# Optimization experiments

Hardware: AMD Instinct MI355X
Metric: run time of the kernel (lower is better)

Reference implementation:

```python
import jax, jax.numpy as jnp
import numpy as np

B, S, D = 64, 1024, 800      # batch, seq_len, encoder hidden (2*hidden_dim, bidirectional)
MS, T = 16, 32               # max slots (spans) per sample, max span length
H = 200                      # LSTM hidden per direction = trs_hidden_dim // 2
NS = 12                      # number of slot names in the domain


def setup_inputs() -> dict:
    key = jax.random.key(0)
    ks = jax.random.split(key, 13)
    s = 0.05
    return {
        "hidden_layers": jax.random.normal(ks[0], (B, S, D), jnp.float32),
        "Wih_f": jax.random.normal(ks[1], (4 * H, D), jnp.float32) * s,
        "Whh_f": jax.random.normal(ks[2], (4 * H, H), jnp.float32) * s,
        "bih_f": jax.random.normal(ks[3], (4 * H,), jnp.float32) * s,
        "bhh_f": jax.random.normal(ks[4], (4 * H,), jnp.float32) * s,
        "Wih_b": jax.random.normal(ks[5], (4 * H, D), jnp.float32) * s,
        "Whh_b": jax.random.normal(ks[6], (4 * H, H), jnp.float32) * s,
        "bih_b": jax.random.normal(ks[7], (4 * H,), jnp.float32) * s,
        "bhh_b": jax.random.normal(ks[8], (4 * H,), jnp.float32) * s,
        "slot_embs": jax.random.normal(ks[9], (2 * H, NS), jnp.float32) * s,
        "span_starts": jnp.sort(jax.random.randint(ks[10], (B, MS), 0, S - T), axis=-1),
        "span_lens": jax.random.randint(ks[11], (B, MS), 1, T + 1),
        "slot_mask": jnp.ones((B, MS), jnp.float32),
    }


def _lstm_scan(x, m, Wih, Whh, bih, bhh):
    """Masked unidirectional LSTM. x: [N,T,Din], m: [N,T] bool-ish. Returns [N,T,H]."""
    N = x.shape[0]
    bias = bih + bhh

    def step(carry, xm):
        h, c = carry
        xt, mt = xm
        z = xt @ Wih.T + h @ Whh.T + bias            # [N, 4H], PyTorch gate order i,f,g,o
        i, f, g, o = jnp.split(z, 4, axis=-1)
        c_new = jax.nn.sigmoid(f) * c + jax.nn.sigmoid(i) * jnp.tanh(g)
        h_new = jax.nn.sigmoid(o) * jnp.tanh(c_new)
        mm = mt[:, None]
        h = jnp.where(mm, h_new, h)                  # freeze state on padded steps
        c = jnp.where(mm, c_new, c)
        return (h, c), h

    h0 = jnp.zeros((N, H), x.dtype)
    (_, _), hs = jax.lax.scan(step, (h0, h0), (jnp.swapaxes(x, 0, 1), m.T.astype(bool)))
    return jnp.swapaxes(hs, 0, 1)


def reference(hidden_layers, Wih_f, Whh_f, bih_f, bhh_f, Wih_b, Whh_b, bih_b, bhh_b,
              slot_embs, span_starts, span_lens, slot_mask):
    Bv, Sv, Dv = hidden_layers.shape
    # Padded ragged span gather: [B, MS, T]
    idx = jnp.clip(span_starts[..., None] + jnp.arange(T), 0, Sv - 1)
    tok_mask = (jnp.arange(T)[None, None, :] < span_lens[..., None]).astype(hidden_layers.dtype)
    spans = hidden_layers[jnp.arange(Bv)[:, None, None], idx]      # [B, MS, T, D]

    x = spans.reshape(Bv * MS, T, Dv)
    m = tok_mask.reshape(Bv * MS, T)
    h_f = _lstm_scan(x, m, Wih_f, Whh_f, bih_f, bhh_f)             # forward direction
    h_b = _lstm_scan(x[:, ::-1], m[:, ::-1], Wih_b, Whh_b, bih_b, bhh_b)[:, ::-1]
    y = jnp.concatenate([h_f, h_b], axis=-1)                       # [N, T, 2H]

    feats = jnp.sum(y * m[..., None], axis=1).reshape(Bv, MS, 2 * H)  # sum over span tokens
    logits = jnp.einsum('bmh,hn->bmn', feats, slot_embs)           # slot-name scores
    return logits * slot_mask[..., None]
```

## Files before the change

### kernel.cpp

```cpp
#include <hip/hip_runtime.h>


typedef __attribute__((ext_vector_type(4))) float f32x4;
typedef __attribute__((ext_vector_type(8))) short s16x8;

__device__ __forceinline__ unsigned short f2bf(float f) {
    union { float f; unsigned int u; } a; a.f = f;
    unsigned int u = a.u;
    u += 0x7fffu + ((u >> 16) & 1u);
    return (unsigned short)(u >> 16);
}
__device__ __forceinline__ float bf2f(unsigned short s) {
    union { unsigned int u; float f; } a; a.u = ((unsigned int)s) << 16; return a.f;
}
__device__ __forceinline__ void async_copy16(const void* g, void* l) {
    __builtin_amdgcn_global_load_lds(
        (const __attribute__((address_space(1))) unsigned int*)g,
        (__attribute__((address_space(3))) unsigned int*)l, 16, 0, 0);
}
__device__ __forceinline__ float sigf_(float x) {
    return 1.f / (1.f + __expf(-x));
}
__device__ __forceinline__ float tanhf_(float x) {
    float ax = fabsf(x);
    float e = __expf(-2.f * ax);
    float r = (1.f - e) / (1.f + e);
    return x < 0.f ? -r : r;
}

__global__ void pack_kernel(const float* __restrict__ Wih_f, const float* __restrict__ Wih_b,
                            const float* __restrict__ Whh_f, const float* __restrict__ Whh_b,
                            const float* __restrict__ bih_f, const float* __restrict__ bhh_f,
                            const float* __restrict__ bih_b, const float* __restrict__ bhh_b,
                            unsigned short* __restrict__ Wp, unsigned short* __restrict__ WhhP,
                            float* __restrict__ biasP)
{
    int tid = blockIdx.x * blockDim.x + threadIdx.x;
    if (tid < 1664 * 800) {
        int n = tid / 800, k = tid - n * 800;
        float v = 0.f;
        if (n < 800)       v = Wih_f[n * 800 + k];
        else if (n < 1600) v = Wih_b[(n - 800) * 800 + k];
        Wp[tid] = f2bf(v);
        return;
    }
    int t2 = tid - 1664 * 800;
    if (t2 < 1600 * 224) {
        int n = t2 / 224, k = t2 - n * 224;
        float v = 0.f;
        if (k < 200) v = (n < 800) ? Whh_f[n * 200 + k] : Whh_b[(n - 800) * 200 + k];
        WhhP[t2] = f2bf(v);
        return;
    }
    int t3 = t2 - 1600 * 224;
    if (t3 < 1664) {
        float v = 0.f;
        if (t3 < 800)       v = bih_f[t3] + bhh_f[t3];
        else if (t3 < 1600) v = bih_b[t3 - 800] + bhh_b[t3 - 800];
        biasP[t3] = v;
    }
}

__global__ void gather_kernel(const float* __restrict__ hidden, const int* __restrict__ starts,
                              unsigned short* __restrict__ Xg)
{
    int tid = blockIdx.x * blockDim.x + threadIdx.x;
    if (tid >= 32768 * 200) return;
    int row = tid / 200;
    int c4  = tid - row * 200;
    int t   = row >> 10, seq = row & 1023;
    int b   = seq >> 4;
    int src = starts[seq] + t;
    src = src < 1023 ? src : 1023;
    const float4 v = *(const float4*)(hidden + (size_t)(b * 1024 + src) * 800 + c4 * 4);
    ushort4 o;
    o.x = f2bf(v.x); o.y = f2bf(v.y); o.z = f2bf(v.z); o.w = f2bf(v.w);
    *(ushort4*)(Xg + (size_t)row * 800 + c4 * 4) = o;
}

__global__ __launch_bounds__(256) void gemm_kernel(const unsigned short* __restrict__ Xg,
                                                   const unsigned short* __restrict__ Wp,
                                                   const float* __restrict__ biasP,
                                                   unsigned short* __restrict__ Zf,
                                                   unsigned short* __restrict__ Zb)
{
    __shared__ __align__(16) unsigned short As[128 * 32];
    __shared__ __align__(16) unsigned short Bs[128 * 32];
    const int tid = threadIdx.x;
    const int wid = tid >> 6, lane = tid & 63;
    const int m0 = blockIdx.x * 128;
    const int n0 = blockIdx.y * 128;
    const int wm = (wid >> 1) * 64, wn = (wid & 1) * 64;
    const int l15 = lane & 15, l4 = lane >> 4;

    f32x4 acc[4][4];
#pragma unroll
    for (int i = 0; i < 4; i++)
#pragma unroll
        for (int j = 0; j < 4; j++) acc[i][j] = (f32x4){0.f, 0.f, 0.f, 0.f};

    const int r0 = tid >> 2,         kc0 = (tid & 3) * 8;
    const int r1 = (256 + tid) >> 2, kc1 = (tid & 3) * 8;
    unsigned short* AsB0 = As + (size_t)(wid * 64) * 8;
    unsigned short* AsB1 = As + (size_t)(256 + wid * 64) * 8;
    unsigned short* BsB0 = Bs + (size_t)(wid * 64) * 8;
    unsigned short* BsB1 = Bs + (size_t)(256 + wid * 64) * 8;

    for (int kb = 0; kb < 25; ++kb) {
        const int kk = kb * 32;
        async_copy16(Xg + (size_t)(m0 + r0) * 800 + kk + kc0, AsB0);
        async_copy16(Xg + (size_t)(m0 + r1) * 800 + kk + kc1, AsB1);
        async_copy16(Wp + (size_t)(n0 + r0) * 800 + kk + kc0, BsB0);
        async_copy16(Wp + (size_t)(n0 + r1) * 800 + kk + kc1, BsB1);
        __syncthreads();

        s16x8 a[4], b[4];
#pragma unroll
        for (int i = 0; i < 4; i++)
            a[i] = *(const s16x8*)(As + (wm + i * 16 + l15) * 32 + l4 * 8);
#pragma unroll
        for (int i = 0; i < 4; i++)
            b[i] = *(const s16x8*)(Bs + (wn + i * 16 + l15) * 32 + l4 * 8);
#pragma unroll
        for (int im = 0; im < 4; im++)
#pragma unroll
            for (int in = 0; in < 4; in++)
                acc[im][in] = __builtin_amdgcn_mfma_f32_16x16x32_bf16(a[im], b[in], acc[im][in], 0, 0, 0);
        __syncthreads();
    }

    float bias_v[4];
#pragma unroll
    for (int in = 0; in < 4; in++) bias_v[in] = biasP[n0 + wn + in * 16 + l15];

#pragma unroll
    for (int im = 0; im < 4; im++) {
        int mbase = m0 + wm + im * 16 + l4 * 4;
#pragma unroll
        for (int in = 0; in < 4; in++) {
            int col = n0 + wn + in * 16 + l15;
            if (col < 1600) {
                int d = col >= 800;
                int u = col - d * 800;
                unsigned short* Zd = d ? Zb : Zf;
#pragma unroll
                for (int r = 0; r < 4; r++)
                    Zd[(size_t)(mbase + r) * 832 + u] = f2bf(acc[im][in][r] + bias_v[in]);
            }
        }
    }
}

__global__ __launch_bounds__(512) void lstm_kernel(const unsigned short* __restrict__ Zf,
                                                   const unsigned short* __restrict__ Zb,
                                                   const unsigned short* __restrict__ WhhP,
                                                   const int* __restrict__ span_lens,
                                                   float* __restrict__ feats)
{
    __shared__ __align__(16) unsigned short h_lds[16 * 232];
    __shared__ __align__(16) unsigned short zbuf[2][16 * 832];
    __shared__ float zm[16 * 812];

    const int bx = blockIdx.x;
    const int dir = bx >> 6;
    const int g = bx & 63;
    const int tid = threadIdx.x;
    const int w = tid >> 6, lane = tid & 63;
    const int l15 = lane & 15, l4 = lane >> 4;
    const unsigned short* __restrict__ Zd = dir ? Zb : Zf;

    for (int i = tid; i < 16 * 232; i += 512) h_lds[i] = 0;

    float c_reg[7], f_reg[7];
    int zmo[7], zbo[7], ho[7], lenk[7], srow[7], ucol[7];
#pragma unroll
    for (int k = 0; k < 7; k++) {
        c_reg[k] = 0.f; f_reg[k] = 0.f;
        int p = tid + k * 512;
        if (p < 3200) {
            int s = p / 200, u = p - s * 200;
            srow[k] = s; ucol[k] = u;
            zmo[k] = s * 812 + u;
            zbo[k] = s * 832 + u;
            ho[k]  = s * 232 + u;
            lenk[k] = span_lens[g * 16 + s];
        } else { zmo[k] = 0; zbo[k] = 0; ho[k] = 0; lenk[k] = -1; srow[k] = 0; ucol[k] = 0; }
    }

    {
        const int t0 = dir ? 31 : 0;
        const unsigned short* gb = Zd + (size_t)(t0 * 1024 + g * 16) * 832;
        for (int c = w; c < 26; c += 8)
            async_copy16(gb + c * 512 + lane * 8, (unsigned short*)zbuf[0] + c * 512);
    }
    __syncthreads();

    for (int step = 0; step < 32; ++step) {
        const int t = dir ? (31 - step) : step;
        const int cur = step & 1, nxt = cur ^ 1;
        if (step < 31) {
            const int tn = dir ? (t - 1) : (t + 1);
            const unsigned short* gb = Zd + (size_t)(tn * 1024 + g * 16) * 832;
            for (int c = w; c < 26; c += 8)
                async_copy16(gb + c * 512 + lane * 8, (unsigned short*)zbuf[nxt] + c * 512);
        }
        for (int j = w; j < 50; j += 8) {
            const int colg = dir * 800 + j * 16 + l15;
            const unsigned short* wrow = WhhP + (size_t)colg * 224 + l4 * 8;
            const unsigned short* hrow = h_lds + l15 * 232 + l4 * 8;
            f32x4 acc0 = (f32x4){0.f, 0.f, 0.f, 0.f};
            f32x4 acc1 = (f32x4){0.f, 0.f, 0.f, 0.f};
#pragma unroll
            for (int kk = 0; kk < 7; ++kk) {
                s16x8 a = *(const s16x8*)(hrow + kk * 32);
                s16x8 b = *(const s16x8*)(wrow + kk * 32);
                if (kk & 1) acc1 = __builtin_amdgcn_mfma_f32_16x16x32_bf16(a, b, acc1, 0, 0, 0);
                else        acc0 = __builtin_amdgcn_mfma_f32_16x16x32_bf16(a, b, acc0, 0, 0, 0);
            }
            f32x4 accs = acc0 + acc1;
#pragma unroll
            for (int r = 0; r < 4; ++r)
                zm[(l4 * 4 + r) * 812 + j * 16 + l15] = accs[r];
        }
        __syncthreads();
#pragma unroll
        for (int k = 0; k < 7; ++k) {
            if (t < lenk[k]) {
                float zi = zm[zmo[k]]       + bf2f(zbuf[cur][zbo[k]]);
                float zf = zm[zmo[k] + 200] + bf2f(zbuf[cur][zbo[k] + 200]);
                float zg = zm[zmo[k] + 400] + bf2f(zbuf[cur][zbo[k] + 400]);
                float zo = zm[zmo[k] + 600] + bf2f(zbuf[cur][zbo[k] + 600]);
                float cn = sigf_(zf) * c_reg[k] + sigf_(zi) * tanhf_(zg);
                float hn = sigf_(zo) * tanhf_(cn);
                c_reg[k] = cn;
                f_reg[k] += hn;
                h_lds[ho[k]] = f2bf(hn);
            }
        }
        __syncthreads();
    }

#pragma unroll
    for (int k = 0; k < 7; ++k)
        if (lenk[k] >= 0)
            feats[(size_t)(g * 16 + srow[k]) * 400 + dir * 200 + ucol[k]] = f_reg[k];
}

__global__ void logits_kernel(const float* __restrict__ feats, const float* __restrict__ se,
                              const float* __restrict__ slot_mask, float* __restrict__ out)
{
    int tid = blockIdx.x * blockDim.x + threadIdx.x;
    if (tid >= 1024 * 12) return;
    int n = tid / 12, ns = tid - n * 12;
    const float* f = feats + (size_t)n * 400;
    float acc = 0.f;
    for (int u = 0; u < 400; ++u) acc += f[u] * se[u * 12 + ns];
    out[tid] = acc * slot_mask[n];
}

extern "C" void kernel_launch(void* const* d_in, const int* in_sizes, int n_in,
                              void* d_out, int out_size, void* d_ws, size_t ws_size,
                              hipStream_t stream)
{
    const float* hidden      = (const float*)d_in[0];
    const float* Wih_f       = (const float*)d_in[1];
    const float* Whh_f       = (const float*)d_in[2];
    const float* bih_f       = (const float*)d_in[3];
    const float* bhh_f       = (const float*)d_in[4];
    const float* Wih_b       = (const float*)d_in[5];
    const float* Whh_b       = (const float*)d_in[6];
    const float* bih_b       = (const float*)d_in[7];
    const float* bhh_b       = (const float*)d_in[8];
    const float* slot_embs   = (const float*)d_in[9];
    const int*   span_starts = (const int*)d_in[10];
    const int*   span_lens   = (const int*)d_in[11];
    const float* slot_mask   = (const float*)d_in[12];
    float* out = (float*)d_out;

    char* ws = (char*)d_ws;
    unsigned short* Xg    = (unsigned short*)(ws + 0);
    unsigned short* Wp    = (unsigned short*)(ws + 52428800);
    unsigned short* WhhP  = (unsigned short*)(ws + 55091200);
    float*          biasP = (float*)         (ws + 55808000);
    unsigned short* Zf    = (unsigned short*)(ws + 55814656);
    unsigned short* Zb    = (unsigned short*)(ws + 110340608);
    float*          feats = (float*)         (ws + 164866560);

    {
        int total = 1664 * 800 + 1600 * 224 + 1664;
        int blocks = (total + 255) / 256;
        pack_kernel<<<blocks, 256, 0, stream>>>(Wih_f, Wih_b, Whh_f, Whh_b,
                                                bih_f, bhh_f, bih_b, bhh_b,
                                                Wp, WhhP, biasP);
    }
    gather_kernel<<<25600, 256, 0, stream>>>(hidden, span_starts, Xg);
    gemm_kernel<<<dim3(256, 13), 256, 0, stream>>>(Xg, Wp, biasP, Zf, Zb);
    lstm_kernel<<<128, 512, 0, stream>>>(Zf, Zb, WhhP, span_lens, feats);
    logits_kernel<<<48, 256, 0, stream>>>(feats, slot_embs, slot_mask, out);
}
```

Baseline: 703.1 us.

## Keep recurrent weights in registers and vectorize LSTM gate update

Each wave now preloads three 16-column tiles of the recurrent weight matrix into registers once, instead of re-reading them from global memory every timestep. The hidden-state A fragments are loaded from LDS once per step and reused across all tiles. The gate update is also regrouped so each thread handles four consecutive units with vector LDS reads and writes, and the zm row stride is padded to 816 for 16-byte alignment. The cost is much higher register use (about 84 VGPRs of weight fragments), and the added occupancy hint in the launch bounds may force spilling.

```diff
diff --git a/kernel.cpp b/kernel.cpp
--- a/kernel.cpp
+++ b/kernel.cpp
@@ -151,15 +151,15 @@
     }
 }
 
-__global__ __launch_bounds__(512) void lstm_kernel(const unsigned short* __restrict__ Zf,
-                                                   const unsigned short* __restrict__ Zb,
-                                                   const unsigned short* __restrict__ WhhP,
-                                                   const int* __restrict__ span_lens,
-                                                   float* __restrict__ feats)
+__global__ __launch_bounds__(512, 2) void lstm_kernel(const unsigned short* __restrict__ Zf,
+                                                      const unsigned short* __restrict__ Zb,
+                                                      const unsigned short* __restrict__ WhhP,
+                                                      const int* __restrict__ span_lens,
+                                                      float* __restrict__ feats)
 {
     __shared__ __align__(16) unsigned short h_lds[16 * 232];
     __shared__ __align__(16) unsigned short zbuf[2][16 * 832];
-    __shared__ float zm[16 * 812];
+    __shared__ __align__(16) float zm[16 * 816];
 
     const int bx = blockIdx.x;
     const int dir = bx >> 6;
@@ -169,22 +169,30 @@
     const int l15 = lane & 15, l4 = lane >> 4;
     const unsigned short* __restrict__ Zd = dir ? Zb : Zf;
 
+    s16x8 breg[3][7];
+#pragma unroll
+    for (int rt = 0; rt < 3; ++rt) {
+        const int colg = dir * 800 + (w * 3 + rt) * 16 + l15;
+        const unsigned short* wrow = WhhP + (size_t)colg * 224 + l4 * 8;
+#pragma unroll
+        for (int kk = 0; kk < 7; ++kk)
+            breg[rt][kk] = *(const s16x8*)(wrow + kk * 32);
+    }
+
     for (int i = tid; i < 16 * 232; i += 512) h_lds[i] = 0;
 
-    float c_reg[7], f_reg[7];
-    int zmo[7], zbo[7], ho[7], lenk[7], srow[7], ucol[7];
-#pragma unroll
-    for (int k = 0; k < 7; k++) {
-        c_reg[k] = 0.f; f_reg[k] = 0.f;
-        int p = tid + k * 512;
-        if (p < 3200) {
-            int s = p / 200, u = p - s * 200;
-            srow[k] = s; ucol[k] = u;
-            zmo[k] = s * 812 + u;
-            zbo[k] = s * 832 + u;
-            ho[k]  = s * 232 + u;
-            lenk[k] = span_lens[g * 16 + s];
-        } else { zmo[k] = 0; zbo[k] = 0; ho[k] = 0; lenk[k] = -1; srow[k] = 0; ucol[k] = 0; }
+    f32x4 c_st[2], f_st[2];
+    int s_g[2], u4_g[2], len_g[2], valid[2];
+#pragma unroll
+    for (int q = 0; q < 2; ++q) {
+        c_st[q] = (f32x4){0.f, 0.f, 0.f, 0.f};
+        f_st[q] = (f32x4){0.f, 0.f, 0.f, 0.f};
+        int grp = tid + q * 512;
+        valid[q] = (grp < 800);
+        int s = valid[q] ? (grp / 50) : 0;
+        int u4 = valid[q] ? (grp - s * 50) : 0;
+        s_g[q] = s; u4_g[q] = u4;
+        len_g[q] = valid[q] ? span_lens[g * 16 + s] : -1;
     }
 
     {
@@ -204,46 +212,83 @@
             for (int c = w; c < 26; c += 8)
                 async_copy16(gb + c * 512 + lane * 8, (unsigned short*)zbuf[nxt] + c * 512);
         }
-        for (int j = w; j < 50; j += 8) {
+
+        s16x8 afr[7];
+        {
+            const unsigned short* hrow = h_lds + l15 * 232 + l4 * 8;
+#pragma unroll
+            for (int kk = 0; kk < 7; ++kk)
+                afr[kk] = *(const s16x8*)(hrow + kk * 32);
+        }
+#pragma unroll
+        for (int rt = 0; rt < 3; ++rt) {
+            f32x4 acc = (f32x4){0.f, 0.f, 0.f, 0.f};
+#pragma unroll
+            for (int kk = 0; kk < 7; ++kk)
+                acc = __builtin_amdgcn_mfma_f32_16x16x32_bf16(afr[kk], breg[rt][kk], acc, 0, 0, 0);
+            const int col = (w * 3 + rt) * 16 + l15;
+#pragma unroll
+            for (int r = 0; r < 4; ++r)
+                zm[(l4 * 4 + r) * 816 + col] = acc[r];
+        }
+        for (int j = 24 + w; j < 50; j += 8) {
             const int colg = dir * 800 + j * 16 + l15;
             const unsigned short* wrow = WhhP + (size_t)colg * 224 + l4 * 8;
-            const unsigned short* hrow = h_lds + l15 * 232 + l4 * 8;
-            f32x4 acc0 = (f32x4){0.f, 0.f, 0.f, 0.f};
-            f32x4 acc1 = (f32x4){0.f, 0.f, 0.f, 0.f};
-#pragma unroll
-            for (int kk = 0; kk < 7; ++kk) {
-                s16x8 a = *(const s16x8*)(hrow + kk * 32);
-                s16x8 b = *(const s16x8*)(wrow + kk * 32);
-                if (kk & 1) acc1 = __builtin_amdgcn_mfma_f32_16x16x32_bf16(a, b, acc1, 0, 0, 0);
-                else        acc0 = __builtin_amdgcn_mfma_f32_16x16x32_bf16(a, b, acc0, 0, 0, 0);
+            s16x8 bs[7];
+#pragma unroll
+            for (int kk = 0; kk < 7; ++kk)
+                bs[kk] = *(const s16x8*)(wrow + kk * 32);
+            f32x4 acc = (f32x4){0.f, 0.f, 0.f, 0.f};
+#pragma unroll
+            for (int kk = 0; kk < 7; ++kk)
+                acc = __builtin_amdgcn_mfma_f32_16x16x32_bf16(afr[kk], bs[kk], acc, 0, 0, 0);
+#pragma unroll
+            for (int r = 0; r < 4; ++r)
+                zm[(l4 * 4 + r) * 816 + j * 16 + l15] = acc[r];
+        }
+        __syncthreads();
+
+#pragma unroll
+        for (int q = 0; q < 2; ++q) {
+            if (valid[q] && t < len_g[q]) {
+                const int s = s_g[q], u4 = u4_g[q];
+                const float* zr = zm + s * 816 + u4 * 4;
+                f32x4 zi = *(const f32x4*)(zr);
+                f32x4 zf = *(const f32x4*)(zr + 200);
+                f32x4 zg = *(const f32x4*)(zr + 400);
+                f32x4 zo = *(const f32x4*)(zr + 600);
+                const unsigned short* zb = zbuf[cur] + s * 832 + u4 * 4;
+                ushort4 bi = *(const ushort4*)(zb);
+                ushort4 bf = *(const ushort4*)(zb + 200);
+                ushort4 bg = *(const ushort4*)(zb + 400);
+                ushort4 bo = *(const ushort4*)(zb + 600);
+                zi[0] += bf2f(bi.x); zi[1] += bf2f(bi.y); zi[2] += bf2f(bi.z); zi[3] += bf2f(bi.w);
+                zf[0] += bf2f(bf.x); zf[1] += bf2f(bf.y); zf[2] += bf2f(bf.z); zf[3] += bf2f(bf.w);
+                zg[0] += bf2f(bg.x); zg[1] += bf2f(bg.y); zg[2] += bf2f(bg.z); zg[3] += bf2f(bg.w);
+                zo[0] += bf2f(bo.x); zo[1] += bf2f(bo.y); zo[2] += bf2f(bo.z); zo[3] += bf2f(bo.w);
+                f32x4 cn, hn;
+#pragma unroll
+                for (int r = 0; r < 4; ++r) {
+                    cn[r] = sigf_(zf[r]) * c_st[q][r] + sigf_(zi[r]) * tanhf_(zg[r]);
+                    hn[r] = sigf_(zo[r]) * tanhf_(cn[r]);
+                }
+                c_st[q] = cn;
+                f_st[q] += hn;
+                ushort4 hp;
+                hp.x = f2bf(hn[0]); hp.y = f2bf(hn[1]); hp.z = f2bf(hn[2]); hp.w = f2bf(hn[3]);
+                *(ushort4*)(h_lds + s * 232 + u4 * 4) = hp;
             }
-            f32x4 accs = acc0 + acc1;
-#pragma unroll
-            for (int r = 0; r < 4; ++r)
-                zm[(l4 * 4 + r) * 812 + j * 16 + l15] = accs[r];
         }
         __syncthreads();
-#pragma unroll
-        for (int k = 0; k < 7; ++k) {
-            if (t < lenk[k]) {
-                float zi = zm[zmo[k]]       + bf2f(zbuf[cur][zbo[k]]);
-                float zf = zm[zmo[k] + 200] + bf2f(zbuf[cur][zbo[k] + 200]);
-                float zg = zm[zmo[k] + 400] + bf2f(zbuf[cur][zbo[k] + 400]);
-                float zo = zm[zmo[k] + 600] + bf2f(zbuf[cur][zbo[k] + 600]);
-                float cn = sigf_(zf) * c_reg[k] + sigf_(zi) * tanhf_(zg);
-                float hn = sigf_(zo) * tanhf_(cn);
-                c_reg[k] = cn;
-                f_reg[k] += hn;
-                h_lds[ho[k]] = f2bf(hn);
-            }
-        }
-        __syncthreads();
-    }
-
-#pragma unroll
-    for (int k = 0; k < 7; ++k)
-        if (lenk[k] >= 0)
-            feats[(size_t)(g * 16 + srow[k]) * 400 + dir * 200 + ucol[k]] = f_reg[k];
+    }
+
+#pragma unroll
+    for (int q = 0; q < 2; ++q) {
+        if (valid[q]) {
+            float* fp = feats + (size_t)(g * 16 + s_g[q]) * 400 + dir * 200 + u4_g[q] * 4;
+            *(f32x4*)fp = f_st[q];
+        }
+    }
 }
 
 __global__ void logits_kernel(const float* __restrict__ feats, const float* __restrict__ se,
```

Measured after the change: 641.4 us. 1.1x faster.
